# Performance work log

Measured on AMD Instinct MI355X. Metric: run time of the kernel, lower is better.

The kernel has to match this reference:

```python
import jax, jax.numpy as jnp
import numpy as np

B, S, D, H = 4, 2048, 1024, 16
HD = D // H  # 64


def setup_inputs() -> dict:
    key = jax.random.key(0)
    ks = jax.random.split(key, 5)
    s = 1.0 / np.sqrt(D)
    return {
        "x": jax.random.normal(ks[0], (B, S, D), dtype=jnp.float32),
        "W_attn": jax.random.normal(ks[1], (D, 3 * D), dtype=jnp.float32) * s,
        "b_attn": jnp.zeros((3 * D,), dtype=jnp.float32),
        "W_proj": jax.random.normal(ks[2], (D, D), dtype=jnp.float32) * s,
        "b_proj": jnp.zeros((D,), dtype=jnp.float32),
    }


def reference(x, W_attn, b_attn, W_proj, b_proj):
    Bx, Sx, Dx = x.shape
    qkv = x @ W_attn + b_attn                      # [B,S,3D]
    q, k, v = jnp.split(qkv, 3, axis=-1)
    q = q.reshape(Bx, Sx, H, HD).transpose(0, 2, 1, 3)  # [B,H,S,hd]
    k = k.reshape(Bx, Sx, H, HD).transpose(0, 2, 1, 3)
    v = v.reshape(Bx, Sx, H, HD).transpose(0, 2, 1, 3)
    att = jnp.einsum('bhqd,bhkd->bhqk', q, k) * (HD ** -0.5)
    causal = jnp.tril(jnp.ones((Sx, Sx), dtype=bool))
    att = jnp.where(causal[None, None], att, -jnp.inf)
    att = jax.nn.softmax(att, axis=-1)
    y = jnp.einsum('bhqk,bhkd->bhqd', att, v)      # [B,H,S,hd]
    y = y.transpose(0, 2, 1, 3).reshape(Bx, Sx, Dx)
    return y @ W_proj + b_proj
```

## Files before the change

kernel.cpp:

```cpp
#include <hip/hip_runtime.h>
#include <hip/hip_bf16.h>
#include <math.h>


typedef __bf16 bf16;
typedef __bf16 bf16x8 __attribute__((ext_vector_type(8)));
typedef __bf16 bf16x4 __attribute__((ext_vector_type(4)));
typedef float f32x4 __attribute__((ext_vector_type(4)));

#define B_ 4
#define S_ 2048
#define D_ 1024
#define H_ 16
#define HD_ 64
#define QSCALE 0.1803368801f

#if __has_builtin(__builtin_amdgcn_exp2f)
#define EXP2F(x) __builtin_amdgcn_exp2f(x)
#else
#define EXP2F(x) exp2f(x)
#endif
#if __has_builtin(__builtin_amdgcn_rcpf)
#define RCPF(x) __builtin_amdgcn_rcpf(x)
#else
#define RCPF(x) (1.0f / (x))
#endif

#define GLOAD_LDS16(gptr, lptr)                                              \
    __builtin_amdgcn_global_load_lds(                                        \
        (const __attribute__((address_space(1))) void*)(uintptr_t)(gptr),    \
        (__attribute__((address_space(3))) void*)(uintptr_t)(lptr), 16, 0, 0)

__global__ void k_cvt(const float* __restrict__ in, bf16* __restrict__ out, int n) {
    int i = (blockIdx.x * 256 + threadIdx.x) * 4;
    if (i >= n) return;
    float4 v = *reinterpret_cast<const float4*>(in + i);
    bf16x4 o;
    o.x = (bf16)v.x; o.y = (bf16)v.y; o.z = (bf16)v.z; o.w = (bf16)v.w;
    *reinterpret_cast<bf16x4*>(out + i) = o;
}

__global__ void k_transpose_cvt(const float* __restrict__ W, bf16* __restrict__ WT,
                                int K, int N) {
    __shared__ float t[32][33];
    int n0 = blockIdx.x * 32, k0 = blockIdx.y * 32;
    int tx = threadIdx.x & 31, ty = threadIdx.x >> 5;
#pragma unroll
    for (int j = 0; j < 32; j += 8)
        t[ty + j][tx] = W[(size_t)(k0 + ty + j) * N + n0 + tx];
    __syncthreads();
#pragma unroll
    for (int j = 0; j < 32; j += 8)
        WT[(size_t)(n0 + ty + j) * K + k0 + tx] = (bf16)t[tx][ty + j];
}

template <int MODE>
__global__ __launch_bounds__(512, 4) void k_gemm(
    const bf16* __restrict__ A, const bf16* __restrict__ BT,
    const float* __restrict__ bias,
    void* out0, void* out1, void* out2, int M, int N, int K) {
    __shared__ __align__(16) bf16 Asm[2][128][64];
    __shared__ __align__(16) bf16 Bsm[2][128][64];
    int mb = blockIdx.y * 128, nb = blockIdx.x * 128;
    int tid = threadIdx.x;
    int w = tid >> 6, lane = tid & 63, lo = lane & 15, qu = lane >> 4;
    int wm = (w >> 2) * 64, wn = (w & 3) * 32;
    int srow = lane >> 3, sch = lane & 7;
    int gch = (sch ^ srow) * 8;
    int r0 = w * 16;

    f32x4 zero = {0.f, 0.f, 0.f, 0.f};
    f32x4 acc[4][2];
#pragma unroll
    for (int i = 0; i < 4; i++)
#pragma unroll
        for (int j = 0; j < 2; j++) acc[i][j] = zero;

    const int nt = K >> 6;

    auto stage = [&](int t, int buf) {
        int kb = t * 64;
#pragma unroll
        for (int g = 0; g < 2; g++) {
            int row = r0 + g * 8;
            GLOAD_LDS16(A + (size_t)(mb + row + srow) * K + kb + gch,
                        &Asm[buf][row][0]);
            GLOAD_LDS16(BT + (size_t)(nb + row + srow) * K + kb + gch,
                        &Bsm[buf][row][0]);
        }
    };

    stage(0, 0);

    for (int t = 0; t < nt; t++) {
        int cur = t & 1;
        if (t + 1 < nt) {
            stage(t + 1, cur ^ 1);
            asm volatile("s_waitcnt vmcnt(4)" ::: "memory");
        } else {
            asm volatile("s_waitcnt vmcnt(0)" ::: "memory");
        }
        __builtin_amdgcn_s_barrier();
        asm volatile("" ::: "memory");
        bf16x8 af[4][2], bfr[2][2];
#pragma unroll
        for (int tt = 0; tt < 4; tt++)
#pragma unroll
            for (int ks = 0; ks < 2; ks++)
                af[tt][ks] = *reinterpret_cast<const bf16x8*>(
                    &Asm[cur][wm + tt * 16 + lo][((ks * 4 + qu) ^ (lo & 7)) * 8]);
#pragma unroll
        for (int j = 0; j < 2; j++)
#pragma unroll
            for (int ks = 0; ks < 2; ks++)
                bfr[j][ks] = *reinterpret_cast<const bf16x8*>(
                    &Bsm[cur][wn + j * 16 + lo][((ks * 4 + qu) ^ (lo & 7)) * 8]);
        __builtin_amdgcn_s_setprio(1);
#pragma unroll
        for (int i = 0; i < 4; i++)
#pragma unroll
            for (int j = 0; j < 2; j++) {
                acc[i][j] = __builtin_amdgcn_mfma_f32_16x16x32_bf16(
                    af[i][0], bfr[j][0], acc[i][j], 0, 0, 0);
                acc[i][j] = __builtin_amdgcn_mfma_f32_16x16x32_bf16(
                    af[i][1], bfr[j][1], acc[i][j], 0, 0, 0);
            }
        __builtin_amdgcn_s_setprio(0);
        asm volatile("" ::: "memory");
        __builtin_amdgcn_s_barrier();
        asm volatile("" ::: "memory");
    }

#pragma unroll
    for (int i = 0; i < 4; i++) {
#pragma unroll
        for (int j = 0; j < 2; j++) {
            int col = nb + wn + j * 16 + lo;
            float bv = bias[col];
            float v4v[4];
#pragma unroll
            for (int r = 0; r < 4; r++) v4v[r] = acc[i][j][r] + bv;
            int row0 = mb + wm + i * 16 + qu * 4;
            if (MODE == 0) {
                int b = row0 >> 11, s0 = row0 & 2047;
                int which = col >> 10, rem = col & 1023;
                int h = rem >> 6, d = rem & 63;
                int bh = b * H_ + h;
                if (which == 2) {
                    bf16x4 pk;
#pragma unroll
                    for (int r = 0; r < 4; r++) pk[r] = (bf16)v4v[r];
                    *reinterpret_cast<bf16x4*>(
                        (bf16*)out2 + ((size_t)bh * HD_ + d) * S_ + s0) = pk;
                } else {
                    bf16* dst = which == 0 ? (bf16*)out0 : (bf16*)out1;
                    float sc = which == 0 ? QSCALE : 1.0f;
#pragma unroll
                    for (int r = 0; r < 4; r++)
                        dst[((size_t)bh * S_ + s0 + r) * HD_ + d] = (bf16)(v4v[r] * sc);
                }
            } else {
#pragma unroll
                for (int r = 0; r < 4; r++)
                    ((float*)out0)[(size_t)(row0 + r) * N + col] = v4v[r];
            }
        }
    }
}

__global__ __launch_bounds__(512, 4) void k_attn(
    const bf16* __restrict__ Q, const bf16* __restrict__ K,
    const bf16* __restrict__ Vt, bf16* __restrict__ Y) {
    __shared__ __align__(16) bf16 Ks[2][64][64];
    __shared__ __align__(16) bf16 Vs[2][64][64];
    __shared__ __align__(16) bf16 Psm[8][32][68];
    int blk = blockIdx.x;
    int bh = blk & 63;
    int praw = blk >> 6;
    int jb8 = praw < 4 ? 7 - praw : praw - 4;
    int tid = threadIdx.x, w = tid >> 6, lane = tid & 63;
    int lo = lane & 15, qu = lane >> 4;
    int b = bh >> 4, h = bh & 15;
    int qbase = jb8 * 256 + w * 32;
    int nt = 4 * jb8 + 4;
    const bf16* Qb = Q + (size_t)bh * S_ * HD_;
    const bf16* Kb = K + (size_t)bh * S_ * HD_;
    const bf16* Vb = Vt + (size_t)bh * HD_ * S_;

    bf16x8 qf[2][2];
#pragma unroll
    for (int i = 0; i < 2; i++)
#pragma unroll
        for (int ks = 0; ks < 2; ks++)
            qf[i][ks] = *reinterpret_cast<const bf16x8*>(
                Qb + (size_t)(qbase + i * 16 + lo) * HD_ + ks * 32 + qu * 8);

    bf16x8 onesf;
#pragma unroll
    for (int j = 0; j < 8; j++) onesf[j] = (bf16)1.0f;

    f32x4 zero = {0.f, 0.f, 0.f, 0.f};
    f32x4 o[2][4];
    f32x4 lacc[2];
#pragma unroll
    for (int i = 0; i < 2; i++) {
        lacc[i] = zero;
#pragma unroll
        for (int r = 0; r < 4; r++) o[i][r] = zero;
    }

    int r0 = w * 8;
    int lrow = lane >> 3, lch = lane & 7;
    int gch = (lch ^ lrow) * 8;

    auto stageKV = [&](int t, int buf) {
        int kb = t * 64;
        GLOAD_LDS16(Kb + (size_t)(kb + r0 + lrow) * HD_ + gch, &Ks[buf][r0][0]);
        GLOAD_LDS16(Vb + (size_t)(r0 + lrow) * S_ + kb + gch, &Vs[buf][r0][0]);
    };

    stageKV(0, 0);

    for (int t = 0; t < nt; t++) {
        int cur = t & 1;
        if (t + 1 < nt) {
            stageKV(t + 1, cur ^ 1);
            asm volatile("s_waitcnt vmcnt(2)" ::: "memory");
        } else {
            asm volatile("s_waitcnt vmcnt(0)" ::: "memory");
        }
        __builtin_amdgcn_s_barrier();
        asm volatile("" ::: "memory");
        int kb = t * 64;
        if (kb <= qbase + 31) {
            bf16x8 kf[4][2];
#pragma unroll
            for (int kc = 0; kc < 4; kc++)
#pragma unroll
                for (int ks = 0; ks < 2; ks++)
                    kf[kc][ks] = *reinterpret_cast<const bf16x8*>(
                        &Ks[cur][kc * 16 + lo][((ks * 4 + qu) ^ (lo & 7)) * 8]);
            f32x4 st[4][2];
            __builtin_amdgcn_s_setprio(1);
#pragma unroll
            for (int kc = 0; kc < 4; kc++)
#pragma unroll
                for (int i = 0; i < 2; i++) {
                    f32x4 a = __builtin_amdgcn_mfma_f32_16x16x32_bf16(
                        kf[kc][0], qf[i][0], zero, 0, 0, 0);
                    st[kc][i] = __builtin_amdgcn_mfma_f32_16x16x32_bf16(
                        kf[kc][1], qf[i][1], a, 0, 0, 0);
                }
            __builtin_amdgcn_s_setprio(0);
            if (kb + 63 > qbase) {
#pragma unroll
                for (int kc = 0; kc < 4; kc++) {
                    int key = kb + kc * 16 + qu * 4;
#pragma unroll
                    for (int i = 0; i < 2; i++) {
                        int q = qbase + i * 16 + lo;
#pragma unroll
                        for (int r = 0; r < 4; r++)
                            st[kc][i][r] = (key + r > q) ? -1e30f : st[kc][i][r];
                    }
                }
            }
#pragma unroll
            for (int kc = 0; kc < 4; kc++)
#pragma unroll
                for (int i = 0; i < 2; i++)
#pragma unroll
                    for (int r = 0; r < 4; r++)
                        st[kc][i][r] = EXP2F(st[kc][i][r]);
#pragma unroll
            for (int i = 0; i < 2; i++)
#pragma unroll
                for (int kc = 0; kc < 4; kc++) {
                    bf16x4 pk;
#pragma unroll
                    for (int r = 0; r < 4; r++) pk[r] = (bf16)st[kc][i][r];
                    *reinterpret_cast<bf16x4*>(
                        &Psm[w][i * 16 + lo][kc * 16 + qu * 4]) = pk;
                }
            asm volatile("s_waitcnt lgkmcnt(0)" ::: "memory");
            bf16x8 pa[2][2];
#pragma unroll
            for (int i = 0; i < 2; i++)
#pragma unroll
                for (int ks = 0; ks < 2; ks++)
                    pa[i][ks] = *reinterpret_cast<const bf16x8*>(
                        &Psm[w][i * 16 + lo][ks * 32 + qu * 8]);
            bf16x8 vfr[4][2];
#pragma unroll
            for (int nc = 0; nc < 4; nc++)
#pragma unroll
                for (int ks = 0; ks < 2; ks++)
                    vfr[nc][ks] = *reinterpret_cast<const bf16x8*>(
                        &Vs[cur][nc * 16 + lo][((ks * 4 + qu) ^ (lo & 7)) * 8]);
            __builtin_amdgcn_s_setprio(1);
#pragma unroll
            for (int i = 0; i < 2; i++) {
                lacc[i] = __builtin_amdgcn_mfma_f32_16x16x32_bf16(
                    pa[i][0], onesf, lacc[i], 0, 0, 0);
                lacc[i] = __builtin_amdgcn_mfma_f32_16x16x32_bf16(
                    pa[i][1], onesf, lacc[i], 0, 0, 0);
            }
#pragma unroll
            for (int nc = 0; nc < 4; nc++)
#pragma unroll
                for (int i = 0; i < 2; i++) {
                    o[i][nc] = __builtin_amdgcn_mfma_f32_16x16x32_bf16(
                        pa[i][0], vfr[nc][0], o[i][nc], 0, 0, 0);
                    o[i][nc] = __builtin_amdgcn_mfma_f32_16x16x32_bf16(
                        pa[i][1], vfr[nc][1], o[i][nc], 0, 0, 0);
                }
            __builtin_amdgcn_s_setprio(0);
        }
        asm volatile("" ::: "memory");
        __builtin_amdgcn_s_barrier();
        asm volatile("" ::: "memory");
    }

#pragma unroll
    for (int i = 0; i < 2; i++) {
#pragma unroll
        for (int r = 0; r < 4; r++) {
            float inv = RCPF(lacc[i][r]);
            int s = qbase + i * 16 + qu * 4 + r;
#pragma unroll
            for (int nc = 0; nc < 4; nc++) {
                float v = o[i][nc][r] * inv;
                Y[((size_t)(b * S_ + s) * H_ + h) * HD_ + nc * 16 + lo] = (bf16)v;
            }
        }
    }
}

extern "C" void kernel_launch(void* const* d_in, const int* in_sizes, int n_in,
                              void* d_out, int out_size, void* d_ws, size_t ws_size,
                              hipStream_t stream) {
    const float* x      = (const float*)d_in[0];
    const float* W_attn = (const float*)d_in[1];
    const float* b_attn = (const float*)d_in[2];
    const float* W_proj = (const float*)d_in[3];
    const float* b_proj = (const float*)d_in[4];
    float* out = (float*)d_out;

    char* ws = (char*)d_ws;
    size_t off = 0;
    auto alloc = [&](size_t bytes) -> void* {
        void* p = ws + off;
        off += (bytes + 255) & ~(size_t)255;
        return p;
    };
    const size_t MD = (size_t)B_ * S_ * D_;
    bf16* xb  = (bf16*)alloc(MD * 2);
    bf16* wta = (bf16*)alloc((size_t)3 * D_ * D_ * 2);
    bf16* wtp = (bf16*)alloc((size_t)D_ * D_ * 2);
    bf16* Qb  = (bf16*)alloc(MD * 2);
    bf16* Kb  = (bf16*)alloc(MD * 2);
    bf16* Vtb = (bf16*)alloc(MD * 2);
    bf16* Ya  = (bf16*)alloc(MD * 2);

    k_cvt<<<8192, 256, 0, stream>>>(x, xb, (int)MD);
    k_transpose_cvt<<<dim3(96, 32), 256, 0, stream>>>(W_attn, wta, D_, 3 * D_);
    k_transpose_cvt<<<dim3(32, 32), 256, 0, stream>>>(W_proj, wtp, D_, D_);
    k_gemm<0><<<dim3(24, 64), 512, 0, stream>>>(xb, wta, b_attn, Qb, Kb, Vtb,
                                                B_ * S_, 3 * D_, D_);
    k_attn<<<dim3(512), 512, 0, stream>>>(Qb, Kb, Vtb, Ya);
    k_gemm<1><<<dim3(8, 64), 512, 0, stream>>>(Ya, wtp, b_proj, out, nullptr, nullptr,
                                               B_ * S_, D_, D_);
}
```

Before: 237.7 us.

## Halve attention query tile per block to double grid size

The attention kernel now gives each wave 16 query rows instead of 32, so a block covers 128 queries and the grid doubles to 1024 blocks. Blocks are ordered longest-first by mapping the block index to query tile 15 down to 0. The aim is better occupancy and load balance across compute units and fewer registers per thread. In exchange, each K/V tile loaded into LDS is reused by half as many queries, which raises K/V global traffic and the per-MFMA overhead of loads and barriers.

New measurement: 231.8 us. 1.03x faster.

```diff
diff --git a/kernel.cpp b/kernel.cpp
--- a/kernel.cpp
+++ b/kernel.cpp
@@ -173,41 +173,34 @@
     const bf16* __restrict__ Vt, bf16* __restrict__ Y) {
     __shared__ __align__(16) bf16 Ks[2][64][64];
     __shared__ __align__(16) bf16 Vs[2][64][64];
-    __shared__ __align__(16) bf16 Psm[8][32][68];
+    __shared__ __align__(16) bf16 Psm[8][16][68];
     int blk = blockIdx.x;
     int bh = blk & 63;
-    int praw = blk >> 6;
-    int jb8 = praw < 4 ? 7 - praw : praw - 4;
+    int jb = 15 - (blk >> 6);
     int tid = threadIdx.x, w = tid >> 6, lane = tid & 63;
     int lo = lane & 15, qu = lane >> 4;
     int b = bh >> 4, h = bh & 15;
-    int qbase = jb8 * 256 + w * 32;
-    int nt = 4 * jb8 + 4;
+    int qbase = jb * 128 + w * 16;
+    int nt = 2 * jb + 2;
     const bf16* Qb = Q + (size_t)bh * S_ * HD_;
     const bf16* Kb = K + (size_t)bh * S_ * HD_;
     const bf16* Vb = Vt + (size_t)bh * HD_ * S_;
 
-    bf16x8 qf[2][2];
-#pragma unroll
-    for (int i = 0; i < 2; i++)
-#pragma unroll
-        for (int ks = 0; ks < 2; ks++)
-            qf[i][ks] = *reinterpret_cast<const bf16x8*>(
-                Qb + (size_t)(qbase + i * 16 + lo) * HD_ + ks * 32 + qu * 8);
+    bf16x8 qf[2];
+#pragma unroll
+    for (int ks = 0; ks < 2; ks++)
+        qf[ks] = *reinterpret_cast<const bf16x8*>(
+            Qb + (size_t)(qbase + lo) * HD_ + ks * 32 + qu * 8);
 
     bf16x8 onesf;
 #pragma unroll
     for (int j = 0; j < 8; j++) onesf[j] = (bf16)1.0f;
 
     f32x4 zero = {0.f, 0.f, 0.f, 0.f};
-    f32x4 o[2][4];
-    f32x4 lacc[2];
-#pragma unroll
-    for (int i = 0; i < 2; i++) {
-        lacc[i] = zero;
-#pragma unroll
-        for (int r = 0; r < 4; r++) o[i][r] = zero;
-    }
+    f32x4 o[4];
+    f32x4 lacc = zero;
+#pragma unroll
+    for (int r = 0; r < 4; r++) o[r] = zero;
 
     int r0 = w * 8;
     int lrow = lane >> 3, lch = lane & 7;
@@ -232,7 +225,7 @@
         __builtin_amdgcn_s_barrier();
         asm volatile("" ::: "memory");
         int kb = t * 64;
-        if (kb <= qbase + 31) {
+        if (kb <= qbase + 15) {
             bf16x8 kf[4][2];
 #pragma unroll
             for (int kc = 0; kc < 4; kc++)
@@ -240,56 +233,45 @@
                 for (int ks = 0; ks < 2; ks++)
                     kf[kc][ks] = *reinterpret_cast<const bf16x8*>(
                         &Ks[cur][kc * 16 + lo][((ks * 4 + qu) ^ (lo & 7)) * 8]);
-            f32x4 st[4][2];
+            f32x4 st[4];
             __builtin_amdgcn_s_setprio(1);
 #pragma unroll
-            for (int kc = 0; kc < 4; kc++)
-#pragma unroll
-                for (int i = 0; i < 2; i++) {
-                    f32x4 a = __builtin_amdgcn_mfma_f32_16x16x32_bf16(
-                        kf[kc][0], qf[i][0], zero, 0, 0, 0);
-                    st[kc][i] = __builtin_amdgcn_mfma_f32_16x16x32_bf16(
-                        kf[kc][1], qf[i][1], a, 0, 0, 0);
-                }
+            for (int kc = 0; kc < 4; kc++) {
+                f32x4 a = __builtin_amdgcn_mfma_f32_16x16x32_bf16(
+                    kf[kc][0], qf[0], zero, 0, 0, 0);
+                st[kc] = __builtin_amdgcn_mfma_f32_16x16x32_bf16(
+                    kf[kc][1], qf[1], a, 0, 0, 0);
+            }
             __builtin_amdgcn_s_setprio(0);
             if (kb + 63 > qbase) {
 #pragma unroll
                 for (int kc = 0; kc < 4; kc++) {
                     int key = kb + kc * 16 + qu * 4;
-#pragma unroll
-                    for (int i = 0; i < 2; i++) {
-                        int q = qbase + i * 16 + lo;
-#pragma unroll
-                        for (int r = 0; r < 4; r++)
-                            st[kc][i][r] = (key + r > q) ? -1e30f : st[kc][i][r];
-                    }
+                    int q = qbase + lo;
+#pragma unroll
+                    for (int r = 0; r < 4; r++)
+                        st[kc][r] = (key + r > q) ? -1e30f : st[kc][r];
                 }
             }
 #pragma unroll
             for (int kc = 0; kc < 4; kc++)
 #pragma unroll
-                for (int i = 0; i < 2; i++)
-#pragma unroll
-                    for (int r = 0; r < 4; r++)
-                        st[kc][i][r] = EXP2F(st[kc][i][r]);
-#pragma unroll
-            for (int i = 0; i < 2; i++)
-#pragma unroll
-                for (int kc = 0; kc < 4; kc++) {
-                    bf16x4 pk;
-#pragma unroll
-                    for (int r = 0; r < 4; r++) pk[r] = (bf16)st[kc][i][r];
-                    *reinterpret_cast<bf16x4*>(
-                        &Psm[w][i * 16 + lo][kc * 16 + qu * 4]) = pk;
-                }
+                for (int r = 0; r < 4; r++)
+                    st[kc][r] = EXP2F(st[kc][r]);
+#pragma unroll
+            for (int kc = 0; kc < 4; kc++) {
+                bf16x4 pk;
+#pragma unroll
+                for (int r = 0; r < 4; r++) pk[r] = (bf16)st[kc][r];
+                *reinterpret_cast<bf16x4*>(
+                    &Psm[w][lo][kc * 16 + qu * 4]) = pk;
+            }
             asm volatile("s_waitcnt lgkmcnt(0)" ::: "memory");
-            bf16x8 pa[2][2];
-#pragma unroll
-            for (int i = 0; i < 2; i++)
-#pragma unroll
-                for (int ks = 0; ks < 2; ks++)
-                    pa[i][ks] = *reinterpret_cast<const bf16x8*>(
-                        &Psm[w][i * 16 + lo][ks * 32 + qu * 8]);
+            bf16x8 pa[2];
+#pragma unroll
+            for (int ks = 0; ks < 2; ks++)
+                pa[ks] = *reinterpret_cast<const bf16x8*>(
+                    &Psm[w][lo][ks * 32 + qu * 8]);
             bf16x8 vfr[4][2];
 #pragma unroll
             for (int nc = 0; nc < 4; nc++)
@@ -298,22 +280,17 @@
                     vfr[nc][ks] = *reinterpret_cast<const bf16x8*>(
                         &Vs[cur][nc * 16 + lo][((ks * 4 + qu) ^ (lo & 7)) * 8]);
             __builtin_amdgcn_s_setprio(1);
-#pragma unroll
-            for (int i = 0; i < 2; i++) {
-                lacc[i] = __builtin_amdgcn_mfma_f32_16x16x32_bf16(
-                    pa[i][0], onesf, lacc[i], 0, 0, 0);
-                lacc[i] = __builtin_amdgcn_mfma_f32_16x16x32_bf16(
-                    pa[i][1], onesf, lacc[i], 0, 0, 0);
-            }
-#pragma unroll
-            for (int nc = 0; nc < 4; nc++)
-#pragma unroll
-                for (int i = 0; i < 2; i++) {
-                    o[i][nc] = __builtin_amdgcn_mfma_f32_16x16x32_bf16(
-                        pa[i][0], vfr[nc][0], o[i][nc], 0, 0, 0);
-                    o[i][nc] = __builtin_amdgcn_mfma_f32_16x16x32_bf16(
-                        pa[i][1], vfr[nc][1], o[i][nc], 0, 0, 0);
-                }
+            lacc = __builtin_amdgcn_mfma_f32_16x16x32_bf16(
+                pa[0], onesf, lacc, 0, 0, 0);
+            lacc = __builtin_amdgcn_mfma_f32_16x16x32_bf16(
+                pa[1], onesf, lacc, 0, 0, 0);
+#pragma unroll
+            for (int nc = 0; nc < 4; nc++) {
+                o[nc] = __builtin_amdgcn_mfma_f32_16x16x32_bf16(
+                    pa[0], vfr[nc][0], o[nc], 0, 0, 0);
+                o[nc] = __builtin_amdgcn_mfma_f32_16x16x32_bf16(
+                    pa[1], vfr[nc][1], o[nc], 0, 0, 0);
+            }
             __builtin_amdgcn_s_setprio(0);
         }
         asm volatile("" ::: "memory");
@@ -322,16 +299,13 @@
     }
 
 #pragma unroll
-    for (int i = 0; i < 2; i++) {
-#pragma unroll
-        for (int r = 0; r < 4; r++) {
-            float inv = RCPF(lacc[i][r]);
-            int s = qbase + i * 16 + qu * 4 + r;
-#pragma unroll
-            for (int nc = 0; nc < 4; nc++) {
-                float v = o[i][nc][r] * inv;
-                Y[((size_t)(b * S_ + s) * H_ + h) * HD_ + nc * 16 + lo] = (bf16)v;
-            }
+    for (int r = 0; r < 4; r++) {
+        float inv = RCPF(lacc[r]);
+        int s = qbase + qu * 4 + r;
+#pragma unroll
+        for (int nc = 0; nc < 4; nc++) {
+            float v = o[nc][r] * inv;
+            Y[((size_t)(b * S_ + s) * H_ + h) * HD_ + nc * 16 + lo] = (bf16)v;
         }
     }
 }
@@ -367,7 +341,7 @@
     k_transpose_cvt<<<dim3(32, 32), 256, 0, stream>>>(W_proj, wtp, D_, D_);
     k_gemm<0><<<dim3(24, 64), 512, 0, stream>>>(xb, wta, b_attn, Qb, Kb, Vtb,
                                                 B_ * S_, 3 * D_, D_);
-    k_attn<<<dim3(512), 512, 0, stream>>>(Qb, Kb, Vtb, Ya);
+    k_attn<<<dim3(1024), 512, 0, stream>>>(Qb, Kb, Vtb, Ya);
     k_gemm<1><<<dim3(8, 64), 512, 0, stream>>>(Ya, wtp, b_proj, out, nullptr, nullptr,
                                                B_ * S_, D_, D_);
 }
```
